# Kernel tuning notes

Hardware: AMD Instinct MI355X
Metric: run time of the kernel (lower is better)

## Reference

```python
import jax, jax.numpy as jnp
import numpy as np

B, M, H, NLAYERS = 32768, 32, 64, 4
DIM_IN = (4 + 1) * M  # 160


def prelu(x, a):
    return jnp.where(x >= 0, x, a * x)


def setup_inputs() -> dict:
    key = jax.random.key(0)
    ks = jax.random.split(key, 10)

    x = jax.random.normal(ks[0], (B, M, 4), dtype=jnp.float32)
    pad_mask = jax.random.randint(ks[1], (B, M), 0, 2).astype(bool)

    def lin(k, fan_out, fan_in):
        bound = 1.0 / np.sqrt(fan_in)
        kw, kb = jax.random.split(k)
        W = jax.random.uniform(kw, (fan_out, fan_in), jnp.float32, -bound, bound)
        b = jax.random.uniform(kb, (fan_out,), jnp.float32, -bound, bound)
        return W, b

    W_in, b_in = lin(ks[2], H, DIM_IN)
    a_in = jnp.full((1,), 0.25, jnp.float32)  # PReLU slope

    enc_W, enc_b = [], []
    for i in range(NLAYERS):
        W, b = lin(ks[3 + i], H, H)
        enc_W.append(W)
        enc_b.append(b)
    W_enc = jnp.stack(enc_W)              # [4, 64, 64]
    b_enc = jnp.stack(enc_b)              # [4, 64]
    a_enc = jnp.full((NLAYERS, 1), 0.25, jnp.float32)

    W_out, b_out = lin(ks[8], M, H)       # [32, 64]

    return {"x": x, "pad_mask": pad_mask, "W_in": W_in, "b_in": b_in,
            "a_in": a_in, "W_enc": W_enc, "b_enc": b_enc, "a_enc": a_enc,
            "W_out": W_out, "b_out": b_out}


def reference(x, pad_mask, W_in, b_in, a_in, W_enc, b_enc, a_enc, W_out, b_out):
    # ---- FullyConnectedNetwork: learn per-satellite weights w [B, M] ----
    valid = (~pad_mask).astype(x.dtype)[..., None]          # [B, M, 1]
    feats = jnp.concatenate([x, valid], axis=-1)            # [B, M, 5]
    feats = feats.reshape(feats.shape[0], -1)               # [B, 5*M] (M == max_sats, pad is no-op)

    h = prelu(feats @ W_in.T + b_in, a_in)                  # [B, 64]
    for i in range(NLAYERS):
        h = prelu(h @ W_enc[i].T + b_enc[i], a_enc[i])
    w = h @ W_out.T + b_out                                  # [B, M]

    # ---- Weighted least squares: diag(w) applied as row-scale (same math as diag_embed + bmm) ----
    ones = jnp.ones(x.shape[:2] + (1,), dtype=x.dtype)
    A = jnp.concatenate([-x[:, :, 1:4], ones], axis=-1)      # [B, M, 4]
    r = x[:, :, 0:1]                                         # [B, M, 1]

    WA = w[:, :, None] * A                                   # [B, M, 4]
    Wr = w[:, :, None] * r                                   # [B, M, 1]

    WA_pinv = jnp.linalg.pinv(WA)                            # [B, 4, M]
    out = jnp.matmul(WA_pinv, Wr)[..., 0]                    # [B, 4]
    return out
```

## Files before the change

### kernel.cpp

```cpp
#include <hip/hip_runtime.h>
#include <cstddef>
#include <cstdint>

typedef float f32x4 __attribute__((ext_vector_type(4)));
typedef __bf16 bf16x8 __attribute__((ext_vector_type(8)));

#define MFMA_B16(a, b, c) __builtin_amdgcn_mfma_f32_16x16x32_bf16(a, b, c, 0, 0, 0)

#define OFF_L0   0u
#define OFF_WV   32768u
#define OFF_ENC  40960u
#define OFF_OUT  106496u

#define XB_OFF   0
#define AH_OFF   8192
#define AL_OFF   10240
#define WS_OFF   12288
#define SMEM_SZ  14400

__device__ __forceinline__ int xadr(int e, int b) { return (e << 9) | (b ^ ((e & 7) << 4)); }
__device__ __forceinline__ int aadr(int e, int b) { return (e << 7) | (b ^ ((e & 7) << 4)); }

__global__ __launch_bounds__(256)
void prep_frags(const float* __restrict__ W_in, const float* __restrict__ W_enc,
                const float* __restrict__ W_out, unsigned* __restrict__ P) {
  const int idx = blockIdx.x * 256 + threadIdx.x;
  if (idx >= 28672) return;
  const int t = idx & 3;
  const int lane = (idx >> 2) & 63;
  const int g = lane >> 4, c = lane & 15;
  const int j0 = t << 1;
  int pl;
  float w0, w1;
  if (idx < 8192) {
    const int rest = idx >> 8;
    pl = rest & 1;
    const int nt = (rest >> 1) & 3;
    const int kt = rest >> 3;
    const int n = 4 * c + nt;
    const int k = kt * 32 + g * 8 + j0;
    const int m = k >> 2, q = k & 3;
    w0 = W_in[n * 160 + 5 * m + q];
    w1 = W_in[n * 160 + 5 * m + q + 1];
  } else if (idx < 10240) {
    const int rest = (idx - 8192) >> 8;
    pl = rest & 1;
    const int nt = rest >> 1;
    const int n = 4 * c + nt;
    const int m = g * 8 + j0;
    w0 = W_in[n * 160 + 5 * m + 4];
    w1 = W_in[n * 160 + 5 * (m + 1) + 4];
  } else if (idx < 26624) {
    const int rel = idx - 10240;
    const int l = rel >> 12;
    const int rest = (rel & 4095) >> 8;
    pl = rest & 1;
    const int nt = (rest >> 1) & 3;
    const int kt = rest >> 3;
    const int n = 4 * c + nt;
    const int k = kt * 32 + g * 8 + j0;
    w0 = W_enc[(l * 64 + n) * 64 + k];
    w1 = W_enc[(l * 64 + n) * 64 + k + 1];
  } else {
    const int rel = idx - 26624;
    const int rest = rel >> 8;
    pl = rest & 1;
    const int nt = (rest >> 1) & 1;
    const int kt = rest >> 2;
    const int mcol = 16 * nt + c;
    const int k = kt * 32 + g * 8 + j0;
    w0 = W_out[mcol * 64 + k];
    w1 = W_out[mcol * 64 + k + 1];
  }
  unsigned short u0, u1;
  if (pl == 0) {
    u0 = __builtin_bit_cast(unsigned short, (__bf16)w0);
    u1 = __builtin_bit_cast(unsigned short, (__bf16)w1);
  } else {
    const __bf16 h0 = (__bf16)w0, h1 = (__bf16)w1;
    u0 = __builtin_bit_cast(unsigned short, (__bf16)(w0 - (float)h0));
    u1 = __builtin_bit_cast(unsigned short, (__bf16)(w1 - (float)h1));
  }
  P[idx] = (unsigned)u0 | ((unsigned)u1 << 16);
}

__global__ __launch_bounds__(64)
void wls_mfma(const float* __restrict__ x, const int* __restrict__ pad,
              const float* __restrict__ b_in, const float* __restrict__ a_in,
              const float* __restrict__ b_enc, const float* __restrict__ a_enc,
              const float* __restrict__ b_out, const char* __restrict__ wf,
              float* __restrict__ out) {
  __shared__ __align__(16) unsigned char smem[SMEM_SZ];
  const int lane = threadIdx.x;
  const int g = lane >> 4, c = lane & 15;
  const int ew = blockIdx.x << 4;

  {
    float4 xv[8];
    const char* src = (const char*)x + (size_t)ew * 512 + lane * 16;
    #pragma unroll
    for (int i = 0; i < 8; ++i) xv[i] = *(const float4*)(src + i * 1024);
    #pragma unroll
    for (int i = 0; i < 8; ++i) {
      const int off = i * 1024 + lane * 16;
      *(float4*)(smem + XB_OFF + xadr(off >> 9, off & 511)) = xv[i];
    }
  }
  {
    #pragma unroll
    for (int t = 0; t < 2; ++t) {
      const int el = lane >> 2;
      const int mq = (lane & 3) + (t << 2);
      const int4 pv = *(const int4*)(pad + (size_t)(ew + el) * 32 + (mq << 2));
      const unsigned ONE = 0x3F80u;
      const unsigned u0 = (pv.x ? 0u : ONE) | ((pv.y ? 0u : ONE) << 16);
      const unsigned u1 = (pv.z ? 0u : ONE) | ((pv.w ? 0u : ONE) << 16);
      *(uint2*)(smem + AL_OFF + aadr(el, mq << 3)) = make_uint2(u0, u1);
    }
  }

  auto bfragG = [&](unsigned goff, int slot) -> bf16x8 {
    return *(const bf16x8*)(wf + goff + slot * 1024 + lane * 16);
  };
  auto xfrag = [&](int kt, bf16x8& ah, bf16x8& al) {
    const int b0 = kt * 128 + g * 32;
    const float4 v0 = *(const float4*)(smem + XB_OFF + xadr(c, b0));
    const float4 v1 = *(const float4*)(smem + XB_OFF + xadr(c, b0 + 16));
    const float vv[8] = {v0.x, v0.y, v0.z, v0.w, v1.x, v1.y, v1.z, v1.w};
    #pragma unroll
    for (int j = 0; j < 8; ++j) {
      const __bf16 h = (__bf16)vv[j];
      ah[j] = h;
      al[j] = (__bf16)(vv[j] - (float)h);
    }
  };
  auto act_store = [&](f32x4* a4, float alpha) {
    #pragma unroll
    for (int r = 0; r < 4; ++r) {
      const int e = (g << 2) + r;
      unsigned hu[2], lu[2];
      #pragma unroll
      for (int q = 0; q < 2; ++q) {
        unsigned short hb[2], lb[2];
        #pragma unroll
        for (int s2 = 0; s2 < 2; ++s2) {
          float h = a4[2 * q + s2][r];
          h = (h >= 0.0f) ? h : alpha * h;
          const __bf16 hh = (__bf16)h;
          const __bf16 ll = (__bf16)(h - (float)hh);
          hb[s2] = __builtin_bit_cast(unsigned short, hh);
          lb[s2] = __builtin_bit_cast(unsigned short, ll);
        }
        hu[q] = (unsigned)hb[0] | ((unsigned)hb[1] << 16);
        lu[q] = (unsigned)lb[0] | ((unsigned)lb[1] << 16);
      }
      *(uint2*)(smem + AH_OFF + aadr(e, c * 8)) = make_uint2(hu[0], hu[1]);
      *(uint2*)(smem + AL_OFF + aadr(e, c * 8)) = make_uint2(lu[0], lu[1]);
    }
  };

  f32x4 acc[4];
  #pragma unroll
  for (int nt = 0; nt < 4; ++nt) {
    const float bv = b_in[4 * c + nt];
    f32x4 a = {bv, bv, bv, bv};
    acc[nt] = a;
  }
  #pragma unroll
  for (int kt = 0; kt < 4; ++kt) {
    bf16x8 ah, al;
    xfrag(kt, ah, al);
    #pragma unroll
    for (int nt = 0; nt < 4; ++nt) {
      const bf16x8 bh = bfragG(OFF_L0, (kt * 4 + nt) * 2);
      const bf16x8 bl = bfragG(OFF_L0, (kt * 4 + nt) * 2 + 1);
      acc[nt] = MFMA_B16(ah, bh, acc[nt]);
      acc[nt] = MFMA_B16(ah, bl, acc[nt]);
      acc[nt] = MFMA_B16(al, bh, acc[nt]);
    }
  }
  {
    const bf16x8 va = *(const bf16x8*)(smem + AL_OFF + aadr(c, g * 16));
    #pragma unroll
    for (int nt = 0; nt < 4; ++nt) {
      const bf16x8 bh = bfragG(OFF_WV, nt * 2);
      const bf16x8 bl = bfragG(OFF_WV, nt * 2 + 1);
      acc[nt] = MFMA_B16(va, bh, acc[nt]);
      acc[nt] = MFMA_B16(va, bl, acc[nt]);
    }
  }
  act_store(acc, a_in[0]);

  #pragma unroll
  for (int l = 0; l < 4; ++l) {
    bf16x8 ah0 = *(const bf16x8*)(smem + AH_OFF + aadr(c, g * 16));
    bf16x8 ah1 = *(const bf16x8*)(smem + AH_OFF + aadr(c, 64 + g * 16));
    bf16x8 al0 = *(const bf16x8*)(smem + AL_OFF + aadr(c, g * 16));
    bf16x8 al1 = *(const bf16x8*)(smem + AL_OFF + aadr(c, 64 + g * 16));
    f32x4 a2[4];
    #pragma unroll
    for (int nt = 0; nt < 4; ++nt) {
      const float bv = b_enc[l * 64 + 4 * c + nt];
      f32x4 a = {bv, bv, bv, bv};
      a2[nt] = a;
    }
    #pragma unroll
    for (int kt = 0; kt < 2; ++kt) {
      const bf16x8 Ah = kt ? ah1 : ah0;
      const bf16x8 Al = kt ? al1 : al0;
      #pragma unroll
      for (int nt = 0; nt < 4; ++nt) {
        const bf16x8 bh = bfragG(OFF_ENC + l * 16384, (kt * 4 + nt) * 2);
        const bf16x8 bl = bfragG(OFF_ENC + l * 16384, (kt * 4 + nt) * 2 + 1);
        a2[nt] = MFMA_B16(Ah, bh, a2[nt]);
        a2[nt] = MFMA_B16(Ah, bl, a2[nt]);
        a2[nt] = MFMA_B16(Al, bh, a2[nt]);
      }
    }
    act_store(a2, a_enc[l]);
  }

  f32x4 aw[2];
  #pragma unroll
  for (int nt = 0; nt < 2; ++nt) {
    const float bv = b_out[16 * nt + c];
    f32x4 a = {bv, bv, bv, bv};
    aw[nt] = a;
  }
  #pragma unroll
  for (int kt = 0; kt < 2; ++kt) {
    const bf16x8 oah = *(const bf16x8*)(smem + AH_OFF + aadr(c, kt * 64 + g * 16));
    const bf16x8 oal = *(const bf16x8*)(smem + AL_OFF + aadr(c, kt * 64 + g * 16));
    #pragma unroll
    for (int nt = 0; nt < 2; ++nt) {
      const bf16x8 obh = bfragG(OFF_OUT, (kt * 2 + nt) * 2);
      const bf16x8 obl = bfragG(OFF_OUT, (kt * 2 + nt) * 2 + 1);
      aw[nt] = MFMA_B16(oah, obh, aw[nt]);
      aw[nt] = MFMA_B16(oah, obl, aw[nt]);
      aw[nt] = MFMA_B16(oal, obh, aw[nt]);
    }
  }
  {
    float* ws = (float*)(smem + WS_OFF);
    #pragma unroll
    for (int nt = 0; nt < 2; ++nt)
      #pragma unroll
      for (int r = 0; r < 4; ++r)
        ws[((g << 2) + r) * 33 + 16 * nt + c] = aw[nt][r];
  }

  {
    const int el = lane >> 2;
    const int p = lane & 3;
    const float* ws = (const float*)(smem + WS_OFF);
    float s[14];
    #pragma unroll
    for (int v = 0; v < 14; ++v) s[v] = 0.0f;
    #pragma unroll
    for (int t = 0; t < 8; ++t) {
      const int mm = (p << 3) + t;
      const float w = ws[el * 33 + mm];
      const float4 xv = *(const float4*)(smem + XB_OFF + xadr(el, mm << 4));
      const float r = xv.x;
      const float a1 = -xv.y, a2 = -xv.z, a3 = -xv.w;
      const float ww = w * w;
      const float w1 = ww * a1, w2 = ww * a2, w3 = ww * a3;
      s[0] += w1 * a1;  s[1] += w1 * a2;  s[2] += w1 * a3;  s[3] += w1;
      s[4] += w2 * a2;  s[5] += w2 * a3;  s[6] += w2;
      s[7] += w3 * a3;  s[8] += w3;
      s[9] += ww;
      s[10] += w1 * r;  s[11] += w2 * r;  s[12] += w3 * r;  s[13] += ww * r;
    }
    #pragma unroll
    for (int v = 0; v < 14; ++v) {
      s[v] += __shfl_xor(s[v], 1);
      s[v] += __shfl_xor(s[v], 2);
    }
    float Mt[4][5] = {
      {s[0], s[1], s[2], s[3], s[10]},
      {s[1], s[4], s[5], s[6], s[11]},
      {s[2], s[5], s[7], s[8], s[12]},
      {s[3], s[6], s[8], s[9], s[13]},
    };
    #pragma unroll
    for (int k = 0; k < 3; ++k) {
      const float inv = 1.0f / Mt[k][k];
      #pragma unroll
      for (int r2 = k + 1; r2 < 4; ++r2) {
        const float fk = Mt[r2][k] * inv;
        #pragma unroll
        for (int cc = k + 1; cc < 5; ++cc) Mt[r2][cc] -= fk * Mt[k][cc];
      }
    }
    const float th3 = Mt[3][4] / Mt[3][3];
    const float th2 = (Mt[2][4] - Mt[2][3] * th3) / Mt[2][2];
    const float th1 = (Mt[1][4] - Mt[1][3] * th3 - Mt[1][2] * th2) / Mt[1][1];
    const float th0 = (Mt[0][4] - Mt[0][3] * th3 - Mt[0][2] * th2 - Mt[0][1] * th1) / Mt[0][0];
    if (p == 0) {
      *(float4*)(out + (size_t)(ew + el) * 4) = make_float4(th0, th1, th2, th3);
    }
  }
}

extern "C" void kernel_launch(void* const* d_in, const int* in_sizes, int n_in,
                              void* d_out, int out_size, void* d_ws, size_t ws_size,
                              hipStream_t stream) {
  const float* x     = (const float*)d_in[0];
  const int*   pad   = (const int*)d_in[1];
  const float* W_in  = (const float*)d_in[2];
  const float* b_in  = (const float*)d_in[3];
  const float* a_in  = (const float*)d_in[4];
  const float* W_enc = (const float*)d_in[5];
  const float* b_enc = (const float*)d_in[6];
  const float* a_enc = (const float*)d_in[7];
  const float* W_out = (const float*)d_in[8];
  const float* b_out = (const float*)d_in[9];
  float* out = (float*)d_out;

  prep_frags<<<112, 256, 0, stream>>>(W_in, W_enc, W_out, (unsigned*)d_ws);
  wls_mfma<<<2048, 64, 0, stream>>>(x, pad, b_in, a_in, b_enc, a_enc, b_out,
                                    (const char*)d_ws, out);
}
```

Measured before the change: 96.71 us.

## Double-buffer weight fragment loads in registers across MLP layers

Replaces per-MFMA global weight fragment loads with two register buffers of eight fragments each. The next stage's weights are loaded while the current stage's MFMAs run, overlapping global/L2 latency with compute. All bias and PReLU slope scalars are hoisted to the kernel start. Launch bounds now request 2 blocks per CU. The extra live registers may raise VGPR pressure or cause spills.

```diff
diff --git a/kernel.cpp b/kernel.cpp
--- a/kernel.cpp
+++ b/kernel.cpp
@@ -84,7 +84,68 @@
   P[idx] = (unsigned)u0 | ((unsigned)u1 << 16);
 }
 
-__global__ __launch_bounds__(64)
+#define LOADG(R, base) do { \
+  const char* p_ = wf + (base) + lane * 16; \
+  R##0 = *(const bf16x8*)(p_); \
+  R##1 = *(const bf16x8*)(p_ + 1024); \
+  R##2 = *(const bf16x8*)(p_ + 2048); \
+  R##3 = *(const bf16x8*)(p_ + 3072); \
+  R##4 = *(const bf16x8*)(p_ + 4096); \
+  R##5 = *(const bf16x8*)(p_ + 5120); \
+  R##6 = *(const bf16x8*)(p_ + 6144); \
+  R##7 = *(const bf16x8*)(p_ + 7168); \
+} while (0)
+
+#define TILE12(R, ah_, al_) do { \
+  acc0 = MFMA_B16(ah_, R##0, acc0); acc0 = MFMA_B16(ah_, R##1, acc0); acc0 = MFMA_B16(al_, R##0, acc0); \
+  acc1 = MFMA_B16(ah_, R##2, acc1); acc1 = MFMA_B16(ah_, R##3, acc1); acc1 = MFMA_B16(al_, R##2, acc1); \
+  acc2 = MFMA_B16(ah_, R##4, acc2); acc2 = MFMA_B16(ah_, R##5, acc2); acc2 = MFMA_B16(al_, R##4, acc2); \
+  acc3 = MFMA_B16(ah_, R##6, acc3); acc3 = MFMA_B16(ah_, R##7, acc3); acc3 = MFMA_B16(al_, R##6, acc3); \
+} while (0)
+
+#define L0STEP(R, kt) do { \
+  bf16x8 ah_, al_; \
+  xfrag(kt, ah_, al_); \
+  TILE12(R, ah_, al_); \
+} while (0)
+
+#define WVSTEP(R) do { \
+  const bf16x8 va_ = *(const bf16x8*)(smem + AL_OFF + aadr(c, g * 16)); \
+  acc0 = MFMA_B16(va_, R##0, acc0); acc0 = MFMA_B16(va_, R##1, acc0); \
+  acc1 = MFMA_B16(va_, R##2, acc1); acc1 = MFMA_B16(va_, R##3, acc1); \
+  acc2 = MFMA_B16(va_, R##4, acc2); acc2 = MFMA_B16(va_, R##5, acc2); \
+  acc3 = MFMA_B16(va_, R##6, acc3); acc3 = MFMA_B16(va_, R##7, acc3); \
+} while (0)
+
+#define ENCA(R, l) do { \
+  { f32x4 t0_ = {ben[l][0], ben[l][0], ben[l][0], ben[l][0]}; acc0 = t0_; } \
+  { f32x4 t1_ = {ben[l][1], ben[l][1], ben[l][1], ben[l][1]}; acc1 = t1_; } \
+  { f32x4 t2_ = {ben[l][2], ben[l][2], ben[l][2], ben[l][2]}; acc2 = t2_; } \
+  { f32x4 t3_ = {ben[l][3], ben[l][3], ben[l][3], ben[l][3]}; acc3 = t3_; } \
+  const bf16x8 ah_ = *(const bf16x8*)(smem + AH_OFF + aadr(c, g * 16)); \
+  const bf16x8 al_ = *(const bf16x8*)(smem + AL_OFF + aadr(c, g * 16)); \
+  TILE12(R, ah_, al_); \
+} while (0)
+
+#define ENCB(R, l) do { \
+  const bf16x8 ah_ = *(const bf16x8*)(smem + AH_OFF + aadr(c, 64 + g * 16)); \
+  const bf16x8 al_ = *(const bf16x8*)(smem + AL_OFF + aadr(c, 64 + g * 16)); \
+  TILE12(R, ah_, al_); \
+  { f32x4 a4_[4] = {acc0, acc1, acc2, acc3}; act_store(a4_, aen[l]); } \
+} while (0)
+
+#define OUTSTEP(R) do { \
+  const bf16x8 h0_ = *(const bf16x8*)(smem + AH_OFF + aadr(c, g * 16)); \
+  const bf16x8 l0_ = *(const bf16x8*)(smem + AL_OFF + aadr(c, g * 16)); \
+  const bf16x8 h1_ = *(const bf16x8*)(smem + AH_OFF + aadr(c, 64 + g * 16)); \
+  const bf16x8 l1_ = *(const bf16x8*)(smem + AL_OFF + aadr(c, 64 + g * 16)); \
+  wacc0 = MFMA_B16(h0_, R##0, wacc0); wacc0 = MFMA_B16(h0_, R##1, wacc0); wacc0 = MFMA_B16(l0_, R##0, wacc0); \
+  wacc1 = MFMA_B16(h0_, R##2, wacc1); wacc1 = MFMA_B16(h0_, R##3, wacc1); wacc1 = MFMA_B16(l0_, R##2, wacc1); \
+  wacc0 = MFMA_B16(h1_, R##4, wacc0); wacc0 = MFMA_B16(h1_, R##5, wacc0); wacc0 = MFMA_B16(l1_, R##4, wacc0); \
+  wacc1 = MFMA_B16(h1_, R##6, wacc1); wacc1 = MFMA_B16(h1_, R##7, wacc1); wacc1 = MFMA_B16(l1_, R##6, wacc1); \
+} while (0)
+
+__global__ __launch_bounds__(64, 2)
 void wls_mfma(const float* __restrict__ x, const int* __restrict__ pad,
               const float* __restrict__ b_in, const float* __restrict__ a_in,
               const float* __restrict__ b_enc, const float* __restrict__ a_enc,
@@ -95,6 +156,16 @@
   const int g = lane >> 4, c = lane & 15;
   const int ew = blockIdx.x << 4;
 
+  const float bin[4] = {b_in[4 * c], b_in[4 * c + 1], b_in[4 * c + 2], b_in[4 * c + 3]};
+  float ben[4][4];
+  #pragma unroll
+  for (int l = 0; l < 4; ++l)
+    #pragma unroll
+    for (int nt = 0; nt < 4; ++nt) ben[l][nt] = b_enc[l * 64 + 4 * c + nt];
+  const float bo[2] = {b_out[c], b_out[16 + c]};
+  const float ain = a_in[0];
+  const float aen[4] = {a_enc[0], a_enc[1], a_enc[2], a_enc[3]};
+
   {
     float4 xv[8];
     const char* src = (const char*)x + (size_t)ew * 512 + lane * 16;
@@ -119,9 +190,6 @@
     }
   }
 
-  auto bfragG = [&](unsigned goff, int slot) -> bf16x8 {
-    return *(const bf16x8*)(wf + goff + slot * 1024 + lane * 16);
-  };
   auto xfrag = [&](int kt, bf16x8& ah, bf16x8& al) {
     const int b0 = kt * 128 + g * 32;
     const float4 v0 = *(const float4*)(smem + XB_OFF + xadr(c, b0));
@@ -134,7 +202,7 @@
       al[j] = (__bf16)(vv[j] - (float)h);
     }
   };
-  auto act_store = [&](f32x4* a4, float alpha) {
+  auto act_store = [&](const f32x4* a4, float alpha) {
     #pragma unroll
     for (int r = 0; r < 4; ++r) {
       const int e = (g << 2) + r;
@@ -159,94 +227,58 @@
     }
   };
 
-  f32x4 acc[4];
-  #pragma unroll
-  for (int nt = 0; nt < 4; ++nt) {
-    const float bv = b_in[4 * c + nt];
-    f32x4 a = {bv, bv, bv, bv};
-    acc[nt] = a;
-  }
-  #pragma unroll
-  for (int kt = 0; kt < 4; ++kt) {
-    bf16x8 ah, al;
-    xfrag(kt, ah, al);
-    #pragma unroll
-    for (int nt = 0; nt < 4; ++nt) {
-      const bf16x8 bh = bfragG(OFF_L0, (kt * 4 + nt) * 2);
-      const bf16x8 bl = bfragG(OFF_L0, (kt * 4 + nt) * 2 + 1);
-      acc[nt] = MFMA_B16(ah, bh, acc[nt]);
-      acc[nt] = MFMA_B16(ah, bl, acc[nt]);
-      acc[nt] = MFMA_B16(al, bh, acc[nt]);
-    }
-  }
-  {
-    const bf16x8 va = *(const bf16x8*)(smem + AL_OFF + aadr(c, g * 16));
-    #pragma unroll
-    for (int nt = 0; nt < 4; ++nt) {
-      const bf16x8 bh = bfragG(OFF_WV, nt * 2);
-      const bf16x8 bl = bfragG(OFF_WV, nt * 2 + 1);
-      acc[nt] = MFMA_B16(va, bh, acc[nt]);
-      acc[nt] = MFMA_B16(va, bl, acc[nt]);
-    }
-  }
-  act_store(acc, a_in[0]);
-
-  #pragma unroll
-  for (int l = 0; l < 4; ++l) {
-    bf16x8 ah0 = *(const bf16x8*)(smem + AH_OFF + aadr(c, g * 16));
-    bf16x8 ah1 = *(const bf16x8*)(smem + AH_OFF + aadr(c, 64 + g * 16));
-    bf16x8 al0 = *(const bf16x8*)(smem + AL_OFF + aadr(c, g * 16));
-    bf16x8 al1 = *(const bf16x8*)(smem + AL_OFF + aadr(c, 64 + g * 16));
-    f32x4 a2[4];
-    #pragma unroll
-    for (int nt = 0; nt < 4; ++nt) {
-      const float bv = b_enc[l * 64 + 4 * c + nt];
-      f32x4 a = {bv, bv, bv, bv};
-      a2[nt] = a;
-    }
-    #pragma unroll
-    for (int kt = 0; kt < 2; ++kt) {
-      const bf16x8 Ah = kt ? ah1 : ah0;
-      const bf16x8 Al = kt ? al1 : al0;
-      #pragma unroll
-      for (int nt = 0; nt < 4; ++nt) {
-        const bf16x8 bh = bfragG(OFF_ENC + l * 16384, (kt * 4 + nt) * 2);
-        const bf16x8 bl = bfragG(OFF_ENC + l * 16384, (kt * 4 + nt) * 2 + 1);
-        a2[nt] = MFMA_B16(Ah, bh, a2[nt]);
-        a2[nt] = MFMA_B16(Ah, bl, a2[nt]);
-        a2[nt] = MFMA_B16(Al, bh, a2[nt]);
-      }
-    }
-    act_store(a2, a_enc[l]);
-  }
-
-  f32x4 aw[2];
-  #pragma unroll
-  for (int nt = 0; nt < 2; ++nt) {
-    const float bv = b_out[16 * nt + c];
-    f32x4 a = {bv, bv, bv, bv};
-    aw[nt] = a;
-  }
-  #pragma unroll
-  for (int kt = 0; kt < 2; ++kt) {
-    const bf16x8 oah = *(const bf16x8*)(smem + AH_OFF + aadr(c, kt * 64 + g * 16));
-    const bf16x8 oal = *(const bf16x8*)(smem + AL_OFF + aadr(c, kt * 64 + g * 16));
-    #pragma unroll
-    for (int nt = 0; nt < 2; ++nt) {
-      const bf16x8 obh = bfragG(OFF_OUT, (kt * 2 + nt) * 2);
-      const bf16x8 obl = bfragG(OFF_OUT, (kt * 2 + nt) * 2 + 1);
-      aw[nt] = MFMA_B16(oah, obh, aw[nt]);
-      aw[nt] = MFMA_B16(oah, obl, aw[nt]);
-      aw[nt] = MFMA_B16(oal, obh, aw[nt]);
-    }
-  }
+  bf16x8 GA0, GA1, GA2, GA3, GA4, GA5, GA6, GA7;
+  bf16x8 GB0, GB1, GB2, GB3, GB4, GB5, GB6, GB7;
+  f32x4 acc0, acc1, acc2, acc3;
+  {
+    f32x4 t0 = {bin[0], bin[0], bin[0], bin[0]}; acc0 = t0;
+    f32x4 t1 = {bin[1], bin[1], bin[1], bin[1]}; acc1 = t1;
+    f32x4 t2 = {bin[2], bin[2], bin[2], bin[2]}; acc2 = t2;
+    f32x4 t3 = {bin[3], bin[3], bin[3], bin[3]}; acc3 = t3;
+  }
+
+  LOADG(GA, OFF_L0 + 0);
+  LOADG(GB, OFF_L0 + 8192);
+  L0STEP(GA, 0);
+  LOADG(GA, OFF_L0 + 16384);
+  L0STEP(GB, 1);
+  LOADG(GB, OFF_L0 + 24576);
+  L0STEP(GA, 2);
+  LOADG(GA, OFF_WV);
+  L0STEP(GB, 3);
+  LOADG(GB, OFF_ENC + 0);
+  WVSTEP(GA);
+  { f32x4 a4_[4] = {acc0, acc1, acc2, acc3}; act_store(a4_, ain); }
+  LOADG(GA, OFF_ENC + 8192);
+  ENCA(GB, 0);
+  LOADG(GB, OFF_ENC + 16384);
+  ENCB(GA, 0);
+  LOADG(GA, OFF_ENC + 24576);
+  ENCA(GB, 1);
+  LOADG(GB, OFF_ENC + 32768);
+  ENCB(GA, 1);
+  LOADG(GA, OFF_ENC + 40960);
+  ENCA(GB, 2);
+  LOADG(GB, OFF_ENC + 49152);
+  ENCB(GA, 2);
+  LOADG(GA, OFF_ENC + 57344);
+  ENCA(GB, 3);
+  LOADG(GB, OFF_OUT);
+  ENCB(GA, 3);
+
+  f32x4 wacc0, wacc1;
+  {
+    f32x4 t0 = {bo[0], bo[0], bo[0], bo[0]}; wacc0 = t0;
+    f32x4 t1 = {bo[1], bo[1], bo[1], bo[1]}; wacc1 = t1;
+  }
+  OUTSTEP(GB);
   {
     float* ws = (float*)(smem + WS_OFF);
     #pragma unroll
-    for (int nt = 0; nt < 2; ++nt)
-      #pragma unroll
-      for (int r = 0; r < 4; ++r)
-        ws[((g << 2) + r) * 33 + 16 * nt + c] = aw[nt][r];
+    for (int r = 0; r < 4; ++r) {
+      ws[((g << 2) + r) * 33 + c] = wacc0[r];
+      ws[((g << 2) + r) * 33 + 16 + c] = wacc1[r];
+    }
   }
 
   {
```

New measurement: 97.93 us. Within noise of the previous version (+1.3%).
